# Optimization experiments

Hardware: AMD Instinct MI355X
Metric: run time of the kernel (lower is better)

## Reference

```python
import jax, jax.numpy as jnp
import numpy as np

DELTA_VAR = 0.5
DELTA_DIST = 2.0
ALPHA, BETA, GAMMA = 1.0, 1.0, 0.001
EPS = 1e-12  # guards sqrt(0) so vjp stays finite; forward effect negligible


def setup_inputs() -> dict:
    key = jax.random.key(0)
    k1, k2 = jax.random.split(key)
    N, E, H, W, C = 4, 16, 768, 768, 32
    input_ = jax.random.normal(k1, (N, E, H, W), dtype=jnp.float32)
    target = jax.random.randint(k2, (N, H, W), 0, C, dtype=jnp.int64)
    # guarantee labels are consecutive starting at 0 (every label present)
    target = target.at[:, 0, :C].set(jnp.arange(C, dtype=jnp.int64))
    return {"input_": input_, "target": target, "num_instances": C}


def _loss_single(emb, lab, C):
    # emb: [E,H,W], lab: [H,W] int
    E = emb.shape[0]
    emb_f = emb.reshape(E, -1).T          # [P,E]
    lab_f = lab.reshape(-1)               # [P]
    counts = jax.ops.segment_sum(jnp.ones(lab_f.shape, jnp.float32), lab_f, num_segments=C)  # [C]
    sums = jax.ops.segment_sum(emb_f, lab_f, num_segments=C)                                  # [C,E]
    means = sums / counts[:, None]        # cluster means, [C,E]

    # variance term: per-pixel distance to own cluster mean
    d = jnp.sqrt(jnp.maximum(jnp.sum((emb_f - means[lab_f]) ** 2, axis=1), EPS))  # [P]
    hinge = jnp.maximum(d - DELTA_VAR, 0.0) ** 2
    var_per_inst = jax.ops.segment_sum(hinge, lab_f, num_segments=C) / counts      # [C]
    variance_term = jnp.sum(var_per_inst) / C

    # distance term: pairwise hinged repulsion between cluster means
    diff = means[:, None, :] - means[None, :, :]                                   # [C,C,E]
    dist = jnp.sqrt(jnp.maximum(jnp.sum(diff ** 2, axis=2), EPS))                  # [C,C]
    repulsion = 2.0 * DELTA_DIST * (1.0 - jnp.eye(C, dtype=dist.dtype))
    hinged = jnp.maximum(repulsion - dist, 0.0) ** 2
    distance_term = jnp.sum(hinged) / (C * (C - 1))

    # regularizer: mean norm of cluster means
    reg_term = jnp.sum(jnp.sqrt(jnp.maximum(jnp.sum(means ** 2, axis=1), EPS))) / C

    return ALPHA * variance_term + BETA * distance_term + GAMMA * reg_term


def reference(input_, target, num_instances):
    C = int(num_instances)
    losses = jax.vmap(lambda e, l: _loss_single(e, l, C))(input_, target)  # [N]
    return jnp.sum(losses) / input_.shape[0]
```

## Files before the change

kernel.cpp:

```cpp
#include <hip/hip_runtime.h>

#define N_IMG 4
#define E_DIM 16
#define H_DIM 768
#define W_DIM 768
#define P_PIX (H_DIM * W_DIM)
#define C_CL 32

#define DELTA_VAR 0.5f
#define DELTA_DIST 2.0f
#define GAMMA_W 0.001f
#define EPS_F 1e-12f

#define WS_SUMS 0
#define WS_CNT 2048
#define WS_VAR 2176
#define WS_TOTAL 2180

#define TP1 1536
#define CH1 (P_PIX / TP1)
#define TSTRIDE 1540
#define STEPS1 (TP1 / 4 / 16)

#define PX2 1024
#define BX2 (P_PIX / PX2)

typedef __attribute__((ext_vector_type(8))) short short8;
typedef __attribute__((ext_vector_type(16))) float float16v;

__device__ __forceinline__ void gatomic_add(float* p, float v) {
#if defined(__HIP_DEVICE_COMPILE__)
  unsafeAtomicAdd(p, v);
#else
  atomicAdd(p, v);
#endif
}

__device__ __forceinline__ short f2bf(float f) {
  return (short)(__float_as_uint(f) >> 16);
}

__global__ __launch_bounds__(256) void pass1(const float* __restrict__ input,
                                             const int* __restrict__ target,
                                             float* __restrict__ ws) {
  __shared__ int s_lab[TP1];
  __shared__ short s_tile[17 * TSTRIDE];
  const int tid = threadIdx.x;
  const int wv = tid >> 6, l = tid & 63;
  const int n = blockIdx.y;
  const int base = blockIdx.x * TP1;
  const int* tgt = target + (size_t)n * P_PIX + base;

  for (int i = tid; i < TP1 / 4; i += 256) {
    *reinterpret_cast<int4*>(&s_lab[i * 4]) =
        *reinterpret_cast<const int4*>(tgt + i * 4);
  }
  for (int i = tid; i < TP1; i += 256)
    s_tile[16 * TSTRIDE + i] = (short)0x3F80;
#pragma unroll
  for (int r = 0; r < 4; ++r) {
    const int row = (wv << 2) + r;
    const float* src = input + ((size_t)n * E_DIM + row) * P_PIX + base;
    float4 v[6];
#pragma unroll
    for (int it = 0; it < 6; ++it)
      v[it] = *reinterpret_cast<const float4*>(src + it * 256 + l * 4);
#pragma unroll
    for (int it = 0; it < 6; ++it) {
      short4 b4;
      b4.x = f2bf(v[it].x);
      b4.y = f2bf(v[it].y);
      b4.z = f2bf(v[it].z);
      b4.w = f2bf(v[it].w);
      *reinterpret_cast<short4*>(&s_tile[row * TSTRIDE + it * 256 + l * 4]) = b4;
    }
  }
  __syncthreads();

  const int m = l & 31;
  const int half = l >> 5;
  const int brow = (m < 17) ? m : 16;
  const short* bbase = &s_tile[brow * TSTRIDE + half * 8];
  const int k0w = wv * (TP1 / 4);
  const short ONE = 0x3F80;

  float16v acc;
#pragma unroll
  for (int i = 0; i < 16; ++i) acc[i] = 0.f;

#pragma unroll
  for (int s = 0; s < STEPS1; ++s) {
    const int k0 = k0w + s * 16;
    const int4 la = *reinterpret_cast<const int4*>(&s_lab[k0 + half * 8]);
    const int4 lb = *reinterpret_cast<const int4*>(&s_lab[k0 + half * 8 + 4]);
    const short4 b0 = *reinterpret_cast<const short4*>(bbase + s * 16);
    const short4 b1 = *reinterpret_cast<const short4*>(bbase + s * 16 + 4);
    short8 a, b;
    a[0] = (la.x == m) ? ONE : 0;
    a[1] = (la.y == m) ? ONE : 0;
    a[2] = (la.z == m) ? ONE : 0;
    a[3] = (la.w == m) ? ONE : 0;
    a[4] = (lb.x == m) ? ONE : 0;
    a[5] = (lb.y == m) ? ONE : 0;
    a[6] = (lb.z == m) ? ONE : 0;
    a[7] = (lb.w == m) ? ONE : 0;
    b[0] = b0.x; b[1] = b0.y; b[2] = b0.z; b[3] = b0.w;
    b[4] = b1.x; b[5] = b1.y; b[6] = b1.z; b[7] = b1.w;
    acc = __builtin_amdgcn_mfma_f32_32x32x16_bf16(a, b, acc, 0, 0, 0);
  }

  __syncthreads();
  float* s_red = reinterpret_cast<float*>(s_tile);
#pragma unroll
  for (int r = 0; r < 16; ++r) s_red[wv * 1024 + r * 64 + l] = acc[r];
  __syncthreads();

  for (int i = tid; i < C_CL * 17; i += 256) {
    const int row = i / 17;
    const int col = i - row * 17;
    const int lane = col | (((row >> 2) & 1) << 5);
    const int reg = (row & 3) | ((row >> 3) << 2);
    const int idx = reg * 64 + lane;
    const float v = s_red[idx] + s_red[1024 + idx] + s_red[2048 + idx] +
                    s_red[3072 + idx];
    if (col < 16)
      gatomic_add(&ws[WS_SUMS + n * C_CL * E_DIM + row * E_DIM + col], v);
    else
      gatomic_add(&ws[WS_CNT + n * C_CL + row], v);
  }
}

__global__ __launch_bounds__(256) void pass2(const float* __restrict__ input,
                                             const int* __restrict__ target,
                                             float* __restrict__ ws) {
  __shared__ float s_mean[C_CL * 17];
  __shared__ float s_invc[C_CL];
  __shared__ float s_red[256];
  const int tid = threadIdx.x;
  const int n = blockIdx.y;
  for (int i = tid; i < C_CL * E_DIM; i += 256) {
    const int c = i >> 4, e = i & 15;
    s_mean[c * 17 + e] =
        ws[WS_SUMS + n * C_CL * E_DIM + i] / ws[WS_CNT + n * C_CL + c];
  }
  if (tid < C_CL) s_invc[tid] = 1.0f / ws[WS_CNT + n * C_CL + tid];
  __syncthreads();

  const int p = blockIdx.x * PX2 + tid * 4;
  const float* inp = input + (size_t)n * E_DIM * P_PIX + p;
  const int4 lab = *reinterpret_cast<const int4*>(target + (size_t)n * P_PIX + p);

  float4 v[E_DIM];
#pragma unroll
  for (int e = 0; e < E_DIM; ++e)
    v[e] = *reinterpret_cast<const float4*>(inp + (size_t)e * P_PIX);

  const float* mx = s_mean + lab.x * 17;
  const float* my = s_mean + lab.y * 17;
  const float* mz = s_mean + lab.z * 17;
  const float* mw = s_mean + lab.w * 17;
  float ax = 0.f, ay = 0.f, az = 0.f, aw = 0.f;
#pragma unroll
  for (int e = 0; e < E_DIM; ++e) {
    const float dx = v[e].x - mx[e];
    const float dy = v[e].y - my[e];
    const float dz = v[e].z - mz[e];
    const float dw = v[e].w - mw[e];
    ax += dx * dx; ay += dy * dy; az += dz * dz; aw += dw * dw;
  }
  float acc = 0.f, d, h;
  d = sqrtf(fmaxf(ax, EPS_F)); h = fmaxf(d - DELTA_VAR, 0.f);
  acc += h * h * s_invc[lab.x];
  d = sqrtf(fmaxf(ay, EPS_F)); h = fmaxf(d - DELTA_VAR, 0.f);
  acc += h * h * s_invc[lab.y];
  d = sqrtf(fmaxf(az, EPS_F)); h = fmaxf(d - DELTA_VAR, 0.f);
  acc += h * h * s_invc[lab.z];
  d = sqrtf(fmaxf(aw, EPS_F)); h = fmaxf(d - DELTA_VAR, 0.f);
  acc += h * h * s_invc[lab.w];

  s_red[tid] = acc;
  __syncthreads();
  for (int s2 = 128; s2 > 0; s2 >>= 1) {
    if (tid < s2) s_red[tid] += s_red[tid + s2];
    __syncthreads();
  }
  if (tid == 0) gatomic_add(&ws[WS_VAR + n], s_red[0]);
}

__global__ __launch_bounds__(256) void finalize(const float* __restrict__ ws,
                                                float* __restrict__ out) {
  __shared__ float s_mean[N_IMG * C_CL * E_DIM];
  __shared__ float red[256];
  const int tid = threadIdx.x;
  for (int i = tid; i < N_IMG * C_CL * E_DIM; i += 256) {
    s_mean[i] = ws[WS_SUMS + i] / ws[WS_CNT + (i >> 4)];
  }
  __syncthreads();

  float acc = 0.f;
  for (int i = tid; i < N_IMG; i += 256) acc += ws[WS_VAR + i] * (1.0f / C_CL);
  for (int i = tid; i < N_IMG * C_CL; i += 256) {
    float nrm2 = 0.f;
    const float* m = s_mean + i * E_DIM;
#pragma unroll
    for (int e = 0; e < E_DIM; ++e) nrm2 += m[e] * m[e];
    acc += GAMMA_W * sqrtf(fmaxf(nrm2, EPS_F)) * (1.0f / C_CL);
  }
  for (int t = tid; t < N_IMG * C_CL * C_CL; t += 256) {
    const int n = t / (C_CL * C_CL);
    const int r = t - n * C_CL * C_CL;
    const int a = r >> 5, b = r & 31;
    if (a != b) {
      const float* ma = s_mean + (n * C_CL + a) * E_DIM;
      const float* mb = s_mean + (n * C_CL + b) * E_DIM;
      float d2 = 0.f;
#pragma unroll
      for (int e = 0; e < E_DIM; ++e) {
        const float df = ma[e] - mb[e];
        d2 += df * df;
      }
      const float dist = sqrtf(fmaxf(d2, EPS_F));
      const float hd = fmaxf(2.f * DELTA_DIST - dist, 0.f);
      acc += hd * hd * (1.0f / (C_CL * (C_CL - 1)));
    }
  }

  red[tid] = acc;
  __syncthreads();
  for (int s = 128; s > 0; s >>= 1) {
    if (tid < s) red[tid] += red[tid + s];
    __syncthreads();
  }
  if (tid == 0) out[0] = red[0] * (1.0f / N_IMG);
}

extern "C" void kernel_launch(void* const* d_in, const int* in_sizes, int n_in,
                              void* d_out, int out_size, void* d_ws,
                              size_t ws_size, hipStream_t stream) {
  const float* input = (const float*)d_in[0];
  const int* target = (const int*)d_in[1];
  float* ws = (float*)d_ws;
  float* out = (float*)d_out;

  hipMemsetAsync(ws, 0, WS_TOTAL * sizeof(float), stream);
  pass1<<<dim3(CH1, N_IMG), 256, 0, stream>>>(input, target, ws);
  pass2<<<dim3(BX2, N_IMG), 256, 0, stream>>>(input, target, ws);
  finalize<<<1, 256, 0, stream>>>(ws, out);
}
```

Measured before the change: 308.1 us.

## Fuse all passes into one persistent kernel with grid barriers

Merges the segment-sum pass, the variance pass and the finalize step into one kernel of 576 blocks that synchronise through atomic-counter grid barriers. Per-block partial sums are written to the workspace and reduced deterministically instead of with float atomics. Each block revisits the same pixel range in the second phase, so that input may still sit in cache. The risk is a deadlock if not all 576 blocks are co-resident (three per CU is assumed), and the serial barrier and reduction steps add latency.

```diff
diff --git a/kernel.cpp b/kernel.cpp
--- a/kernel.cpp
+++ b/kernel.cpp
@@ -2,9 +2,7 @@
 
 #define N_IMG 4
 #define E_DIM 16
-#define H_DIM 768
-#define W_DIM 768
-#define P_PIX (H_DIM * W_DIM)
+#define P_PIX 589824
 #define C_CL 32
 
 #define DELTA_VAR 0.5f
@@ -12,101 +10,102 @@
 #define GAMMA_W 0.001f
 #define EPS_F 1e-12f
 
-#define WS_SUMS 0
-#define WS_CNT 2048
-#define WS_VAR 2176
-#define WS_TOTAL 2180
-
-#define TP1 1536
-#define CH1 (P_PIX / TP1)
-#define TSTRIDE 1540
-#define STEPS1 (TP1 / 4 / 16)
-
-#define PX2 1024
-#define BX2 (P_PIX / PX2)
+#define BPI 144
+#define GRID_B (N_IMG * BPI)
+#define PXB (P_PIX / BPI)
+#define NCH 4
+#define TSTR 1036
+
+#define WS_CTR 0
+#define WS_PART1 16
+#define WS_SUMS (WS_PART1 + GRID_B * 544)
+#define WS_VARP (WS_SUMS + N_IMG * 544)
 
 typedef __attribute__((ext_vector_type(8))) short short8;
 typedef __attribute__((ext_vector_type(16))) float float16v;
 
-__device__ __forceinline__ void gatomic_add(float* p, float v) {
-#if defined(__HIP_DEVICE_COMPILE__)
-  unsafeAtomicAdd(p, v);
-#else
-  atomicAdd(p, v);
-#endif
-}
-
 __device__ __forceinline__ short f2bf(float f) {
   return (short)(__float_as_uint(f) >> 16);
 }
 
-__global__ __launch_bounds__(256) void pass1(const float* __restrict__ input,
-                                             const int* __restrict__ target,
-                                             float* __restrict__ ws) {
-  __shared__ int s_lab[TP1];
-  __shared__ short s_tile[17 * TSTRIDE];
+__device__ __forceinline__ void grid_barrier(int* ctr, int expected) {
+  __syncthreads();
+  if (threadIdx.x == 0) {
+    __threadfence();
+    __hip_atomic_fetch_add(ctr, 1, __ATOMIC_ACQ_REL, __HIP_MEMORY_SCOPE_AGENT);
+    while (__hip_atomic_load(ctr, __ATOMIC_ACQUIRE,
+                             __HIP_MEMORY_SCOPE_AGENT) < expected)
+      __builtin_amdgcn_s_sleep(8);
+  }
+  __syncthreads();
+  __threadfence();
+}
+
+__global__ __launch_bounds__(256, 3) void fused(const float* __restrict__ input,
+                                                const int* __restrict__ target,
+                                                float* __restrict__ ws,
+                                                float* __restrict__ out) {
+  __shared__ short s_tile[17 * TSTR];
+  __shared__ int s_lab[1024];
+  __shared__ float s_mean[C_CL * 17];
+  __shared__ float s_invc[C_CL];
+  __shared__ float s_redB[256];
+  int* ctr = reinterpret_cast<int*>(ws) + WS_CTR;
+
   const int tid = threadIdx.x;
   const int wv = tid >> 6, l = tid & 63;
-  const int n = blockIdx.y;
-  const int base = blockIdx.x * TP1;
-  const int* tgt = target + (size_t)n * P_PIX + base;
-
-  for (int i = tid; i < TP1 / 4; i += 256) {
-    *reinterpret_cast<int4*>(&s_lab[i * 4]) =
-        *reinterpret_cast<const int4*>(tgt + i * 4);
-  }
-  for (int i = tid; i < TP1; i += 256)
-    s_tile[16 * TSTRIDE + i] = (short)0x3F80;
-#pragma unroll
-  for (int r = 0; r < 4; ++r) {
-    const int row = (wv << 2) + r;
-    const float* src = input + ((size_t)n * E_DIM + row) * P_PIX + base;
-    float4 v[6];
-#pragma unroll
-    for (int it = 0; it < 6; ++it)
-      v[it] = *reinterpret_cast<const float4*>(src + it * 256 + l * 4);
-#pragma unroll
-    for (int it = 0; it < 6; ++it) {
+  const int bx = blockIdx.x, n = blockIdx.y;
+  const int g = n * BPI + bx;
+  const int* tgt = target + (size_t)n * P_PIX + bx * PXB;
+  const float* inp = input + (size_t)n * E_DIM * P_PIX + bx * PXB;
+
+  for (int i = tid; i < 1024; i += 256) s_tile[16 * TSTR + i] = (short)0x3F80;
+
+  const int m = l & 31, half = l >> 5;
+  const int brow = (m < 17) ? m : 16;
+  const short ONE = 0x3F80;
+  float16v acc;
+#pragma unroll
+  for (int i = 0; i < 16; ++i) acc[i] = 0.f;
+
+  for (int c = 0; c < NCH; ++c) {
+    const int p = c * 1024 + tid * 4;
+    const int4 lab = *reinterpret_cast<const int4*>(tgt + p);
+    float4 v[E_DIM];
+#pragma unroll
+    for (int e = 0; e < E_DIM; ++e)
+      v[e] = *reinterpret_cast<const float4*>(inp + (size_t)e * P_PIX + p);
+    __syncthreads();
+    *reinterpret_cast<int4*>(&s_lab[tid * 4]) = lab;
+#pragma unroll
+    for (int e = 0; e < E_DIM; ++e) {
       short4 b4;
-      b4.x = f2bf(v[it].x);
-      b4.y = f2bf(v[it].y);
-      b4.z = f2bf(v[it].z);
-      b4.w = f2bf(v[it].w);
-      *reinterpret_cast<short4*>(&s_tile[row * TSTRIDE + it * 256 + l * 4]) = b4;
-    }
-  }
-  __syncthreads();
-
-  const int m = l & 31;
-  const int half = l >> 5;
-  const int brow = (m < 17) ? m : 16;
-  const short* bbase = &s_tile[brow * TSTRIDE + half * 8];
-  const int k0w = wv * (TP1 / 4);
-  const short ONE = 0x3F80;
-
-  float16v acc;
-#pragma unroll
-  for (int i = 0; i < 16; ++i) acc[i] = 0.f;
-
-#pragma unroll
-  for (int s = 0; s < STEPS1; ++s) {
-    const int k0 = k0w + s * 16;
-    const int4 la = *reinterpret_cast<const int4*>(&s_lab[k0 + half * 8]);
-    const int4 lb = *reinterpret_cast<const int4*>(&s_lab[k0 + half * 8 + 4]);
-    const short4 b0 = *reinterpret_cast<const short4*>(bbase + s * 16);
-    const short4 b1 = *reinterpret_cast<const short4*>(bbase + s * 16 + 4);
-    short8 a, b;
-    a[0] = (la.x == m) ? ONE : 0;
-    a[1] = (la.y == m) ? ONE : 0;
-    a[2] = (la.z == m) ? ONE : 0;
-    a[3] = (la.w == m) ? ONE : 0;
-    a[4] = (lb.x == m) ? ONE : 0;
-    a[5] = (lb.y == m) ? ONE : 0;
-    a[6] = (lb.z == m) ? ONE : 0;
-    a[7] = (lb.w == m) ? ONE : 0;
-    b[0] = b0.x; b[1] = b0.y; b[2] = b0.z; b[3] = b0.w;
-    b[4] = b1.x; b[5] = b1.y; b[6] = b1.z; b[7] = b1.w;
-    acc = __builtin_amdgcn_mfma_f32_32x32x16_bf16(a, b, acc, 0, 0, 0);
+      b4.x = f2bf(v[e].x); b4.y = f2bf(v[e].y);
+      b4.z = f2bf(v[e].z); b4.w = f2bf(v[e].w);
+      *reinterpret_cast<short4*>(&s_tile[e * TSTR + tid * 4]) = b4;
+    }
+    __syncthreads();
+    const int k0w = wv * 256;
+#pragma unroll
+    for (int s = 0; s < 16; ++s) {
+      const int k0 = k0w + s * 16 + half * 8;
+      const int4 la = *reinterpret_cast<const int4*>(&s_lab[k0]);
+      const int4 lb = *reinterpret_cast<const int4*>(&s_lab[k0 + 4]);
+      const short4 b0 = *reinterpret_cast<const short4*>(&s_tile[brow * TSTR + k0]);
+      const short4 b1 = *reinterpret_cast<const short4*>(&s_tile[brow * TSTR + k0 + 4]);
+      short8 a, b;
+      a[0] = (la.x == m) ? ONE : 0;
+      a[1] = (la.y == m) ? ONE : 0;
+      a[2] = (la.z == m) ? ONE : 0;
+      a[3] = (la.w == m) ? ONE : 0;
+      a[4] = (lb.x == m) ? ONE : 0;
+      a[5] = (lb.y == m) ? ONE : 0;
+      a[6] = (lb.z == m) ? ONE : 0;
+      a[7] = (lb.w == m) ? ONE : 0;
+      b[0] = b0.x; b[1] = b0.y; b[2] = b0.z; b[3] = b0.w;
+      b[4] = b1.x; b[5] = b1.y; b[6] = b1.z; b[7] = b1.w;
+      acc = __builtin_amdgcn_mfma_f32_32x32x16_bf16(a, b, acc, 0, 0, 0);
+    }
   }
 
   __syncthreads();
@@ -114,105 +113,119 @@
 #pragma unroll
   for (int r = 0; r < 16; ++r) s_red[wv * 1024 + r * 64 + l] = acc[r];
   __syncthreads();
-
+  float* part = ws + WS_PART1 + (size_t)g * 544;
   for (int i = tid; i < C_CL * 17; i += 256) {
-    const int row = i / 17;
-    const int col = i - row * 17;
+    const int row = i / 17, col = i - row * 17;
     const int lane = col | (((row >> 2) & 1) << 5);
     const int reg = (row & 3) | ((row >> 3) << 2);
     const int idx = reg * 64 + lane;
-    const float v = s_red[idx] + s_red[1024 + idx] + s_red[2048 + idx] +
-                    s_red[3072 + idx];
-    if (col < 16)
-      gatomic_add(&ws[WS_SUMS + n * C_CL * E_DIM + row * E_DIM + col], v);
-    else
-      gatomic_add(&ws[WS_CNT + n * C_CL + row], v);
-  }
-}
-
-__global__ __launch_bounds__(256) void pass2(const float* __restrict__ input,
-                                             const int* __restrict__ target,
-                                             float* __restrict__ ws) {
-  __shared__ float s_mean[C_CL * 17];
-  __shared__ float s_invc[C_CL];
-  __shared__ float s_red[256];
-  const int tid = threadIdx.x;
-  const int n = blockIdx.y;
+    part[i] = s_red[idx] + s_red[1024 + idx] + s_red[2048 + idx] +
+              s_red[3072 + idx];
+  }
+
+  grid_barrier(&ctr[0], GRID_B);
+
+  if (bx == 0) {
+    const float* pbase = ws + WS_PART1 + (size_t)n * BPI * 544;
+    float* sums = ws + WS_SUMS + n * 544;
+    for (int i = tid; i < 544; i += 256) {
+      float a2 = 0.f;
+#pragma unroll 8
+      for (int b = 0; b < BPI; ++b) a2 += pbase[(size_t)b * 544 + i];
+      sums[i] = a2;
+    }
+  }
+
+  grid_barrier(&ctr[1], GRID_B);
+
+  const float* sums = ws + WS_SUMS + n * 544;
   for (int i = tid; i < C_CL * E_DIM; i += 256) {
-    const int c = i >> 4, e = i & 15;
-    s_mean[c * 17 + e] =
-        ws[WS_SUMS + n * C_CL * E_DIM + i] / ws[WS_CNT + n * C_CL + c];
-  }
-  if (tid < C_CL) s_invc[tid] = 1.0f / ws[WS_CNT + n * C_CL + tid];
-  __syncthreads();
-
-  const int p = blockIdx.x * PX2 + tid * 4;
-  const float* inp = input + (size_t)n * E_DIM * P_PIX + p;
-  const int4 lab = *reinterpret_cast<const int4*>(target + (size_t)n * P_PIX + p);
-
-  float4 v[E_DIM];
-#pragma unroll
-  for (int e = 0; e < E_DIM; ++e)
-    v[e] = *reinterpret_cast<const float4*>(inp + (size_t)e * P_PIX);
-
-  const float* mx = s_mean + lab.x * 17;
-  const float* my = s_mean + lab.y * 17;
-  const float* mz = s_mean + lab.z * 17;
-  const float* mw = s_mean + lab.w * 17;
-  float ax = 0.f, ay = 0.f, az = 0.f, aw = 0.f;
-#pragma unroll
-  for (int e = 0; e < E_DIM; ++e) {
-    const float dx = v[e].x - mx[e];
-    const float dy = v[e].y - my[e];
-    const float dz = v[e].z - mz[e];
-    const float dw = v[e].w - mw[e];
-    ax += dx * dx; ay += dy * dy; az += dz * dz; aw += dw * dw;
-  }
-  float acc = 0.f, d, h;
-  d = sqrtf(fmaxf(ax, EPS_F)); h = fmaxf(d - DELTA_VAR, 0.f);
-  acc += h * h * s_invc[lab.x];
-  d = sqrtf(fmaxf(ay, EPS_F)); h = fmaxf(d - DELTA_VAR, 0.f);
-  acc += h * h * s_invc[lab.y];
-  d = sqrtf(fmaxf(az, EPS_F)); h = fmaxf(d - DELTA_VAR, 0.f);
-  acc += h * h * s_invc[lab.z];
-  d = sqrtf(fmaxf(aw, EPS_F)); h = fmaxf(d - DELTA_VAR, 0.f);
-  acc += h * h * s_invc[lab.w];
-
-  s_red[tid] = acc;
+    const int c2 = i >> 4, e = i & 15;
+    s_mean[c2 * 17 + e] = sums[c2 * 17 + e] / sums[c2 * 17 + 16];
+  }
+  if (tid < C_CL) s_invc[tid] = 1.0f / sums[tid * 17 + 16];
+  __syncthreads();
+
+  float vacc = 0.f;
+  for (int c = 0; c < NCH; ++c) {
+    const int p = c * 1024 + tid * 4;
+    const int4 lab = *reinterpret_cast<const int4*>(tgt + p);
+    float4 v[E_DIM];
+#pragma unroll
+    for (int e = 0; e < E_DIM; ++e)
+      v[e] = *reinterpret_cast<const float4*>(inp + (size_t)e * P_PIX + p);
+    const float* mx = s_mean + lab.x * 17;
+    const float* my = s_mean + lab.y * 17;
+    const float* mz = s_mean + lab.z * 17;
+    const float* mw = s_mean + lab.w * 17;
+    float ax = 0.f, ay = 0.f, az = 0.f, aw = 0.f;
+#pragma unroll
+    for (int e = 0; e < E_DIM; ++e) {
+      const float dx = v[e].x - mx[e];
+      const float dy = v[e].y - my[e];
+      const float dz = v[e].z - mz[e];
+      const float dw = v[e].w - mw[e];
+      ax += dx * dx; ay += dy * dy; az += dz * dz; aw += dw * dw;
+    }
+    float d, h;
+    d = sqrtf(fmaxf(ax, EPS_F)); h = fmaxf(d - DELTA_VAR, 0.f);
+    vacc += h * h * s_invc[lab.x];
+    d = sqrtf(fmaxf(ay, EPS_F)); h = fmaxf(d - DELTA_VAR, 0.f);
+    vacc += h * h * s_invc[lab.y];
+    d = sqrtf(fmaxf(az, EPS_F)); h = fmaxf(d - DELTA_VAR, 0.f);
+    vacc += h * h * s_invc[lab.z];
+    d = sqrtf(fmaxf(aw, EPS_F)); h = fmaxf(d - DELTA_VAR, 0.f);
+    vacc += h * h * s_invc[lab.w];
+  }
+  s_redB[tid] = vacc;
   __syncthreads();
   for (int s2 = 128; s2 > 0; s2 >>= 1) {
-    if (tid < s2) s_red[tid] += s_red[tid + s2];
-    __syncthreads();
-  }
-  if (tid == 0) gatomic_add(&ws[WS_VAR + n], s_red[0]);
-}
-
-__global__ __launch_bounds__(256) void finalize(const float* __restrict__ ws,
-                                                float* __restrict__ out) {
-  __shared__ float s_mean[N_IMG * C_CL * E_DIM];
-  __shared__ float red[256];
-  const int tid = threadIdx.x;
+    if (tid < s2) s_redB[tid] += s_redB[tid + s2];
+    __syncthreads();
+  }
+  if (tid == 0) ws[WS_VARP + g] = s_redB[0];
+
+  __syncthreads();
+  if (tid == 0) {
+    __threadfence();
+    __hip_atomic_fetch_add(&ctr[2], 1, __ATOMIC_ACQ_REL,
+                           __HIP_MEMORY_SCOPE_AGENT);
+  }
+  if (g != 0) return;
+  if (tid == 0) {
+    while (__hip_atomic_load(&ctr[2], __ATOMIC_ACQUIRE,
+                             __HIP_MEMORY_SCOPE_AGENT) < GRID_B)
+      __builtin_amdgcn_s_sleep(8);
+  }
+  __syncthreads();
+  __threadfence();
+
+  float* s_meanF = reinterpret_cast<float*>(s_tile);
   for (int i = tid; i < N_IMG * C_CL * E_DIM; i += 256) {
-    s_mean[i] = ws[WS_SUMS + i] / ws[WS_CNT + (i >> 4)];
-  }
-  __syncthreads();
-
-  float acc = 0.f;
-  for (int i = tid; i < N_IMG; i += 256) acc += ws[WS_VAR + i] * (1.0f / C_CL);
+    const int nn = i >> 9, rem = i & 511;
+    const int c2 = rem >> 4, e = rem & 15;
+    s_meanF[i] = ws[WS_SUMS + nn * 544 + c2 * 17 + e] /
+                 ws[WS_SUMS + nn * 544 + c2 * 17 + 16];
+  }
+  __syncthreads();
+
+  float acc2 = 0.f;
+  for (int i = tid; i < GRID_B; i += 256)
+    acc2 += ws[WS_VARP + i] * (1.0f / C_CL);
   for (int i = tid; i < N_IMG * C_CL; i += 256) {
     float nrm2 = 0.f;
-    const float* m = s_mean + i * E_DIM;
-#pragma unroll
-    for (int e = 0; e < E_DIM; ++e) nrm2 += m[e] * m[e];
-    acc += GAMMA_W * sqrtf(fmaxf(nrm2, EPS_F)) * (1.0f / C_CL);
+    const float* mm = s_meanF + i * E_DIM;
+#pragma unroll
+    for (int e = 0; e < E_DIM; ++e) nrm2 += mm[e] * mm[e];
+    acc2 += GAMMA_W * sqrtf(fmaxf(nrm2, EPS_F)) * (1.0f / C_CL);
   }
   for (int t = tid; t < N_IMG * C_CL * C_CL; t += 256) {
-    const int n = t / (C_CL * C_CL);
-    const int r = t - n * C_CL * C_CL;
-    const int a = r >> 5, b = r & 31;
-    if (a != b) {
-      const float* ma = s_mean + (n * C_CL + a) * E_DIM;
-      const float* mb = s_mean + (n * C_CL + b) * E_DIM;
+    const int nn = t / (C_CL * C_CL);
+    const int r = t - nn * C_CL * C_CL;
+    const int a2 = r >> 5, b2 = r & 31;
+    if (a2 != b2) {
+      const float* ma = s_meanF + (nn * C_CL + a2) * E_DIM;
+      const float* mb = s_meanF + (nn * C_CL + b2) * E_DIM;
       float d2 = 0.f;
 #pragma unroll
       for (int e = 0; e < E_DIM; ++e) {
@@ -221,17 +234,16 @@
       }
       const float dist = sqrtf(fmaxf(d2, EPS_F));
       const float hd = fmaxf(2.f * DELTA_DIST - dist, 0.f);
-      acc += hd * hd * (1.0f / (C_CL * (C_CL - 1)));
-    }
-  }
-
-  red[tid] = acc;
-  __syncthreads();
-  for (int s = 128; s > 0; s >>= 1) {
-    if (tid < s) red[tid] += red[tid + s];
-    __syncthreads();
-  }
-  if (tid == 0) out[0] = red[0] * (1.0f / N_IMG);
+      acc2 += hd * hd * (1.0f / (C_CL * (C_CL - 1)));
+    }
+  }
+  s_redB[tid] = acc2;
+  __syncthreads();
+  for (int s2 = 128; s2 > 0; s2 >>= 1) {
+    if (tid < s2) s_redB[tid] += s_redB[tid + s2];
+    __syncthreads();
+  }
+  if (tid == 0) out[0] = s_redB[0] * (1.0f / N_IMG);
 }
 
 extern "C" void kernel_launch(void* const* d_in, const int* in_sizes, int n_in,
@@ -242,8 +254,6 @@
   float* ws = (float*)d_ws;
   float* out = (float*)d_out;
 
-  hipMemsetAsync(ws, 0, WS_TOTAL * sizeof(float), stream);
-  pass1<<<dim3(CH1, N_IMG), 256, 0, stream>>>(input, target, ws);
-  pass2<<<dim3(BX2, N_IMG), 256, 0, stream>>>(input, target, ws);
-  finalize<<<1, 256, 0, stream>>>(ws, out);
-}
+  hipMemsetAsync(ws, 0, 64, stream);
+  fused<<<dim3(BPI, N_IMG), 256, 0, stream>>>(input, target, ws, out);
+}
```

New measurement: 698.0 us. 127% more time.
